# Performance work log

Measured on AMD Instinct MI355X. Metric: run time of the kernel, lower is better.

The kernel has to match this reference:

```python
import jax, jax.numpy as jnp
import numpy as np

LEAKY_SLOPE = 0.01

def bilinear_interpolate(grid, coords):
    # grid: [H, W, C]; coords: [N, 2] in [0,1] (x, y order as in torch code)
    H = grid.shape[0] - 1
    W = grid.shape[1] - 1
    fx = coords[:, 0] * W
    fy = coords[:, 1] * H
    x0 = fx.astype(jnp.int32)
    y0 = fy.astype(jnp.int32)
    xf = jnp.mod(fx, 1.0)
    yf = jnp.mod(fy, 1.0)
    x1 = jnp.minimum(x0 + 1, W)
    y1 = jnp.minimum(y0 + 1, H)
    tl = grid[y0, x0]  # [N, C]
    tr = grid[y0, x1]
    bl = grid[y1, x0]
    br = grid[y1, x1]
    xf = xf[:, None]
    yf = yf[:, None]
    top = (1.0 - xf) * tl + xf * tr
    bot = (1.0 - xf) * bl + xf * br
    return (1.0 - yf) * top + yf * bot


def setup_inputs() -> dict:
    key = jax.random.key(0)
    ks = jax.random.split(key, 10)
    N = 2097152
    pos = jax.random.uniform(ks[0], (N, 2), dtype=jnp.float32)
    dir = jax.random.uniform(ks[1], (N, 2), dtype=jnp.float32)
    pos_grid = jax.random.normal(ks[2], (256, 256, 3), dtype=jnp.float32) * 10.0
    dir_grid = jax.random.normal(ks[3], (256, 256, 3), dtype=jnp.float32) * 10.0
    # Linear layers: PyTorch default init U(-1/sqrt(fan_in), 1/sqrt(fan_in))
    def linear(kw, kb, fan_in, fan_out):
        bound = 1.0 / np.sqrt(fan_in)
        W = jax.random.uniform(kw, (fan_out, fan_in), minval=-bound, maxval=bound, dtype=jnp.float32)
        b = jax.random.uniform(kb, (fan_out,), minval=-bound, maxval=bound, dtype=jnp.float32)
        return W, b
    W1, b1 = linear(ks[4], ks[5], 6, 64)
    W2, b2 = linear(ks[6], ks[7], 64, 64)
    W3, b3 = linear(ks[8], ks[9], 64, 1)
    return {"pos": pos, "dir": dir, "pos_grid": pos_grid, "dir_grid": dir_grid,
            "W1": W1, "b1": b1, "W2": W2, "b2": b2, "W3": W3, "b3": b3}


def reference(pos, dir, pos_grid, dir_grid, W1, b1, W2, b2, W3, b3):
    pos_feat = jax.lax.stop_gradient(bilinear_interpolate(pos_grid, pos))  # .detach() in torch
    dir_feat = jax.lax.stop_gradient(bilinear_interpolate(dir_grid, dir))
    x = jnp.concatenate([pos_feat, dir_feat], axis=1)  # [N, 6]
    x = jax.nn.leaky_relu(x @ W1.T + b1, LEAKY_SLOPE)
    x = jax.nn.leaky_relu(x @ W2.T + b2, LEAKY_SLOPE)
    return jax.nn.sigmoid(x @ W3.T + b3)  # [N, 1]
```

## Files before the change

kernel.cpp:

```cpp
#include <hip/hip_runtime.h>
#include <hip/hip_bf16.h>
#include <math.h>


#define NTHREADS 256
#define NB 4

typedef __attribute__((ext_vector_type(8))) short bf16x8;
typedef __attribute__((ext_vector_type(4))) float f32x4;
typedef __attribute__((ext_vector_type(2))) float f32x2;
typedef __attribute__((ext_vector_type(4))) int i32x4;
typedef __attribute__((ext_vector_type(2))) int i32x2;

static __device__ __forceinline__ short f2bf(float f) {
    return __builtin_bit_cast(short, __float2bfloat16(f));
}
static __device__ __forceinline__ int pk2(float lo, float hi) {
    int r;
    asm("v_cvt_pk_bf16_f32 %0, %1, %2" : "=v"(r) : "v"(lo), "v"(hi));
    return r;
}
static __device__ __forceinline__ float bflo(int u) {
    return __builtin_bit_cast(float, u << 16);
}
static __device__ __forceinline__ float bfhi(int u) {
    return __builtin_bit_cast(float, (int)(u & 0xffff0000));
}
static __device__ __forceinline__ f32x2 leaky2(f32x2 x) {
    return __builtin_elementwise_max(x, x * 0.01f);
}
static __device__ __forceinline__ int selperm(int addr, int pa, int pb,
                                              bool hi) {
    int va = __builtin_amdgcn_ds_bpermute(addr, pa);
    int vb = __builtin_amdgcn_ds_bpermute(addr, pb);
    return hi ? vb : va;
}

__global__ __launch_bounds__(256) void make_patches(
    const float* __restrict__ gP, const float* __restrict__ gD,
    int* __restrict__ outP, int* __restrict__ outD) {
    int gid = blockIdx.x * 256 + threadIdx.x;
    const float* g = (gid < 65536) ? gP : gD;
    int* po = (gid < 65536) ? outP : outD;
    int id = gid & 65535;
    int y0 = id >> 8, x0 = id & 255;
    int x1 = min(x0 + 1, 255), y1 = min(y0 + 1, 255);
    const float* tl = g + (y0 * 256 + x0) * 3;
    const float* tr = g + (y0 * 256 + x1) * 3;
    const float* bl = g + (y1 * 256 + x0) * 3;
    const float* br = g + (y1 * 256 + x1) * 3;
    i32x4 u0;
    i32x2 u1;
    u0[0] = pk2(tl[0], bl[0]);
    u0[1] = pk2(tl[1], bl[1]);
    u0[2] = pk2(tl[2], bl[2]);
    u0[3] = pk2(tr[0], br[0]);
    u1[0] = pk2(tr[1], br[1]);
    u1[1] = pk2(tr[2], br[2]);
    *(i32x4*)(po + id * 8) = u0;
    *(i32x2*)(po + id * 8 + 4) = u1;
}

static __device__ __forceinline__ void patch_issue(
    const int* __restrict__ tab, float px, float py, int* P, float& xf,
    float& yf) {
    float fx = px * 255.0f;
    float fy = py * 255.0f;
    int x0 = (int)fx;
    int y0 = (int)fy;
    xf = fx - floorf(fx);
    yf = fy - floorf(fy);
    int idx = (y0 << 8) | x0;
    i32x4 a = *(const i32x4*)(tab + idx * 8);
    i32x2 b = *(const i32x2*)(tab + idx * 8 + 4);
    P[0] = a[0]; P[1] = a[1]; P[2] = a[2];
    P[3] = a[3]; P[4] = b[0]; P[5] = b[1];
}

static __device__ __forceinline__ void patch_lerp(const int* P, float xf,
                                                  float yf, float* f) {
#pragma unroll
    for (int ch = 0; ch < 3; ++ch) {
        f32x2 L2 = {bflo(P[ch]), bfhi(P[ch])};
        f32x2 R2 = {bflo(P[ch + 3]), bfhi(P[ch + 3])};
        f32x2 v = (R2 - L2) * xf + L2;
        f[ch] = fmaf(yf, v.y - v.x, v.x);
    }
}

__global__ __launch_bounds__(NTHREADS, 3) void mlp_mfma_kernel(
    const float* __restrict__ pos, const float* __restrict__ dir,
    const int* __restrict__ patP, const int* __restrict__ patD,
    const float* __restrict__ W1, const float* __restrict__ b1,
    const float* __restrict__ W2, const float* __restrict__ b2,
    const float* __restrict__ W3, const float* __restrict__ b3,
    float* __restrict__ out) {
    const int lane = threadIdx.x & 63;
    const int c = lane & 15;
    const int q = lane >> 4;

    bf16x8 A1f[4];
#pragma unroll
    for (int mt = 0; mt < 4; ++mt) {
        int f = mt * 16 + c;
        bf16x8 t;
#pragma unroll
        for (int j = 0; j < 8; ++j) {
            float v = 0.0f;
            if (q == 0) {
                if (j < 6) v = W1[f * 6 + j];
                else if (j == 6) v = b1[f];
            }
            t[j] = f2bf(v);
        }
        A1f[mt] = t;
    }
    bf16x8 A2f[2][4];
#pragma unroll
    for (int kt = 0; kt < 2; ++kt)
#pragma unroll
        for (int mt = 0; mt < 4; ++mt) {
            int n2 = mt * 16 + c;
            int k0 = kt * 32 + q * 8;
            bf16x8 t;
#pragma unroll
            for (int j = 0; j < 8; ++j) t[j] = f2bf(W2[n2 * 64 + k0 + j]);
            A2f[kt][mt] = t;
        }
    f32x4 ci[4], w3q[4];
#pragma unroll
    for (int mt = 0; mt < 4; ++mt)
#pragma unroll
        for (int r = 0; r < 4; ++r) {
            ci[mt][r] = b2[mt * 16 + q * 4 + r];
            w3q[mt][r] = W3[mt * 16 + q * 4 + r];
        }
    const float b3s = b3[0];
    const int dbias = 0x3F80;
    const f32x4 zacc = {0.f, 0.f, 0.f, 0.f};

    const int exA = ((((q & 1) * 2) * 16) + c) * 4;
    const int exB = exA + 64;
    const bool hi = (q >= 2);

    const long wave_global = (long)(blockIdx.x * 4) + (threadIdx.x >> 6);
    const long base0 = wave_global * (64L * NB);
    const float2* pos2 = (const float2*)pos;
    const float2* dir2 = (const float2*)dir;

    int PA[12];
    float frA[4];
    float2 cp1, cd1;
    {
        float2 c0p = pos2[base0 + lane], c0d = dir2[base0 + lane];
        cp1 = pos2[base0 + 64 + lane];
        cd1 = dir2[base0 + 64 + lane];
        patch_issue(patP, c0p.x, c0p.y, PA, frA[0], frA[1]);
        patch_issue(patD, c0d.x, c0d.y, PA + 6, frA[2], frA[3]);
    }

#pragma unroll 1
    for (int ib = 0; ib < NB; ++ib) {
        const long base = base0 + ib * 64;

        int d0, d1, d2;
        {
            float feat[6];
            patch_lerp(PA, frA[0], frA[1], feat);
            patch_lerp(PA + 6, frA[2], frA[3], feat + 3);
            d0 = pk2(feat[0], feat[1]);
            d1 = pk2(feat[2], feat[3]);
            d2 = pk2(feat[4], feat[5]);
        }

        patch_issue(patP, cp1.x, cp1.y, PA, frA[0], frA[1]);
        patch_issue(patD, cd1.x, cd1.y, PA + 6, frA[2], frA[3]);
        {
            int mb = min(ib + 2, NB - 1);
            cp1 = pos2[base0 + mb * 64 + lane];
            cd1 = dir2[base0 + mb * 64 + lane];
        }

        float s[4];
#pragma unroll
        for (int pt = 0; pt < 4; ++pt) {
            const int fa = (pt * 16 + c) * 4;
            i32x4 bi;
            bi[0] = __builtin_amdgcn_ds_bpermute(fa, d0);
            bi[1] = __builtin_amdgcn_ds_bpermute(fa, d1);
            bi[2] = __builtin_amdgcn_ds_bpermute(fa, d2);
            bi[3] = dbias;
            bf16x8 bfeat = __builtin_bit_cast(bf16x8, bi);

            f32x4 a1[4];
#pragma unroll
            for (int mt = 0; mt < 4; ++mt)
                a1[mt] = __builtin_amdgcn_mfma_f32_16x16x32_bf16(
                    A1f[mt], bfeat, zacc, 0, 0, 0);

            int Pk[4][2];
#pragma unroll
            for (int mt = 0; mt < 4; ++mt) {
                f32x2 p0 = {a1[mt][0], a1[mt][1]};
                f32x2 p1 = {a1[mt][2], a1[mt][3]};
                p0 = leaky2(p0);
                p1 = leaky2(p1);
                Pk[mt][0] = pk2(p0.x, p0.y);
                Pk[mt][1] = pk2(p1.x, p1.y);
            }

            f32x4 a2[4];
#pragma unroll
            for (int kt = 0; kt < 2; ++kt) {
                i32x4 Q;
                Q[0] = selperm(exA, Pk[2 * kt][0], Pk[2 * kt + 1][0], hi);
                Q[1] = selperm(exA, Pk[2 * kt][1], Pk[2 * kt + 1][1], hi);
                Q[2] = selperm(exB, Pk[2 * kt][0], Pk[2 * kt + 1][0], hi);
                Q[3] = selperm(exB, Pk[2 * kt][1], Pk[2 * kt + 1][1], hi);
                bf16x8 bq = __builtin_bit_cast(bf16x8, Q);
#pragma unroll
                for (int mt = 0; mt < 4; ++mt)
                    a2[mt] = __builtin_amdgcn_mfma_f32_16x16x32_bf16(
                        A2f[kt][mt], bq, kt == 0 ? ci[mt] : a2[mt], 0, 0, 0);
            }

            f32x2 accv = {0.f, 0.f};
#pragma unroll
            for (int mt = 0; mt < 4; ++mt) {
                f32x2 x0 = {a2[mt][0], a2[mt][1]};
                f32x2 x1 = {a2[mt][2], a2[mt][3]};
                x0 = leaky2(x0);
                x1 = leaky2(x1);
                f32x2 w0 = {w3q[mt][0], w3q[mt][1]};
                f32x2 w1 = {w3q[mt][2], w3q[mt][3]};
                accv = x0 * w0 + accv;
                accv = x1 * w1 + accv;
            }
            float tt = accv.x + accv.y;
            tt += __shfl_xor(tt, 16, 64);
            tt += __shfl_xor(tt, 32, 64);
            s[pt] = tt;
        }

        float sa = (q & 1) ? s[1] : s[0];
        float sb = (q & 1) ? s[3] : s[2];
        float v = (q & 2) ? sb : sa;
        v += b3s;
        v = 1.0f / (1.0f + __expf(-v));
        out[base + q * 16 + c] = v;
    }
}

extern "C" void kernel_launch(void* const* d_in, const int* in_sizes, int n_in,
                              void* d_out, int out_size, void* d_ws,
                              size_t ws_size, hipStream_t stream) {
    const float* pos = (const float*)d_in[0];
    const float* dir = (const float*)d_in[1];
    const float* pos_grid = (const float*)d_in[2];
    const float* dir_grid = (const float*)d_in[3];
    const float* W1 = (const float*)d_in[4];
    const float* b1 = (const float*)d_in[5];
    const float* W2 = (const float*)d_in[6];
    const float* b2 = (const float*)d_in[7];
    const float* W3 = (const float*)d_in[8];
    const float* b3 = (const float*)d_in[9];
    float* out = (float*)d_out;

    int* patP = (int*)d_ws;
    int* patD = patP + 65536 * 8;

    make_patches<<<512, 256, 0, stream>>>(pos_grid, dir_grid, patP, patD);

    const int n = in_sizes[0] / 2;
    const int batches = n / 64;
    const int waves = batches / NB;
    const int blocks = waves / 4;

    mlp_mfma_kernel<<<blocks, NTHREADS, 0, stream>>>(
        pos, dir, patP, patD, W1, b1, W2, b2, W3, b3, out);
}
```

Measured before the change: 158.1 us.

## Split bilinear feature gathering into a separate kernel writing packed bf16 features

Moves the grid patch gathers and bilinear interpolation out of the MFMA MLP kernel into a new make_feats kernel. It writes packed bf16 feature vectors (with the bias-one slot) to workspace. The MLP kernel then loads these directly in MFMA B-operand layout, which removes the ds_bpermute shuffles and the latency-bound gathers from the compute loop. The cost is an extra kernel launch plus a write and read of 16 bytes per point (about 32 MB each way) through global memory.

```diff
diff --git a/kernel.cpp b/kernel.cpp
--- a/kernel.cpp
+++ b/kernel.cpp
@@ -88,9 +88,33 @@
     }
 }
 
+__global__ __launch_bounds__(256) void make_feats(
+    const float2* __restrict__ pos2, const float2* __restrict__ dir2,
+    const int* __restrict__ patP, const int* __restrict__ patD,
+    i32x4* __restrict__ featpk, int npts) {
+    int i = blockIdx.x * 256 + threadIdx.x;
+    int stride = gridDim.x * 256;
+#pragma unroll 1
+    for (; i < npts; i += stride) {
+        float2 pp = pos2[i], dd = dir2[i];
+        int P[12];
+        float fr[4];
+        patch_issue(patP, pp.x, pp.y, P, fr[0], fr[1]);
+        patch_issue(patD, dd.x, dd.y, P + 6, fr[2], fr[3]);
+        float feat[6];
+        patch_lerp(P, fr[0], fr[1], feat);
+        patch_lerp(P + 6, fr[2], fr[3], feat + 3);
+        i32x4 dv;
+        dv[0] = pk2(feat[0], feat[1]);
+        dv[1] = pk2(feat[2], feat[3]);
+        dv[2] = pk2(feat[4], feat[5]);
+        dv[3] = 0x3F80;
+        featpk[i] = dv;
+    }
+}
+
 __global__ __launch_bounds__(NTHREADS, 3) void mlp_mfma_kernel(
-    const float* __restrict__ pos, const float* __restrict__ dir,
-    const int* __restrict__ patP, const int* __restrict__ patD,
+    const i32x4* __restrict__ featpk,
     const float* __restrict__ W1, const float* __restrict__ b1,
     const float* __restrict__ W2, const float* __restrict__ b2,
     const float* __restrict__ W3, const float* __restrict__ b3,
@@ -136,7 +160,6 @@
             w3q[mt][r] = W3[mt * 16 + q * 4 + r];
         }
     const float b3s = b3[0];
-    const int dbias = 0x3F80;
     const f32x4 zacc = {0.f, 0.f, 0.f, 0.f};
 
     const int exA = ((((q & 1) * 2) * 16) + c) * 4;
@@ -145,52 +168,26 @@
 
     const long wave_global = (long)(blockIdx.x * 4) + (threadIdx.x >> 6);
     const long base0 = wave_global * (64L * NB);
-    const float2* pos2 = (const float2*)pos;
-    const float2* dir2 = (const float2*)dir;
-
-    int PA[12];
-    float frA[4];
-    float2 cp1, cd1;
-    {
-        float2 c0p = pos2[base0 + lane], c0d = dir2[base0 + lane];
-        cp1 = pos2[base0 + 64 + lane];
-        cd1 = dir2[base0 + 64 + lane];
-        patch_issue(patP, c0p.x, c0p.y, PA, frA[0], frA[1]);
-        patch_issue(patD, c0d.x, c0d.y, PA + 6, frA[2], frA[3]);
-    }
+
+    i32x4 bfc[4];
+#pragma unroll
+    for (int pt = 0; pt < 4; ++pt) bfc[pt] = featpk[base0 + pt * 16 + c];
 
 #pragma unroll 1
     for (int ib = 0; ib < NB; ++ib) {
         const long base = base0 + ib * 64;
 
-        int d0, d1, d2;
+        i32x4 bfn[4];
         {
-            float feat[6];
-            patch_lerp(PA, frA[0], frA[1], feat);
-            patch_lerp(PA + 6, frA[2], frA[3], feat + 3);
-            d0 = pk2(feat[0], feat[1]);
-            d1 = pk2(feat[2], feat[3]);
-            d2 = pk2(feat[4], feat[5]);
-        }
-
-        patch_issue(patP, cp1.x, cp1.y, PA, frA[0], frA[1]);
-        patch_issue(patD, cd1.x, cd1.y, PA + 6, frA[2], frA[3]);
-        {
-            int mb = min(ib + 2, NB - 1);
-            cp1 = pos2[base0 + mb * 64 + lane];
-            cd1 = dir2[base0 + mb * 64 + lane];
+            const long nb = base0 + (long)min(ib + 1, NB - 1) * 64;
+#pragma unroll
+            for (int pt = 0; pt < 4; ++pt) bfn[pt] = featpk[nb + pt * 16 + c];
         }
 
         float s[4];
 #pragma unroll
         for (int pt = 0; pt < 4; ++pt) {
-            const int fa = (pt * 16 + c) * 4;
-            i32x4 bi;
-            bi[0] = __builtin_amdgcn_ds_bpermute(fa, d0);
-            bi[1] = __builtin_amdgcn_ds_bpermute(fa, d1);
-            bi[2] = __builtin_amdgcn_ds_bpermute(fa, d2);
-            bi[3] = dbias;
-            bf16x8 bfeat = __builtin_bit_cast(bf16x8, bi);
+            bf16x8 bfeat = __builtin_bit_cast(bf16x8, bfc[pt]);
 
             f32x4 a1[4];
 #pragma unroll
@@ -248,6 +245,9 @@
         v += b3s;
         v = 1.0f / (1.0f + __expf(-v));
         out[base + q * 16 + c] = v;
+
+#pragma unroll
+        for (int pt = 0; pt < 4; ++pt) bfc[pt] = bfn[pt];
     }
 }
 
@@ -266,16 +266,21 @@
     const float* b3 = (const float*)d_in[9];
     float* out = (float*)d_out;
 
+    const int n = in_sizes[0] / 2;
+
     int* patP = (int*)d_ws;
     int* patD = patP + 65536 * 8;
+    i32x4* featpk = (i32x4*)(patD + 65536 * 8);
 
     make_patches<<<512, 256, 0, stream>>>(pos_grid, dir_grid, patP, patD);
-
-    const int n = in_sizes[0] / 2;
+    make_feats<<<2048, 256, 0, stream>>>((const float2*)pos,
+                                         (const float2*)dir, patP, patD,
+                                         featpk, n);
+
     const int batches = n / 64;
     const int waves = batches / NB;
     const int blocks = waves / 4;
 
-    mlp_mfma_kernel<<<blocks, NTHREADS, 0, stream>>>(
-        pos, dir, patP, patD, W1, b1, W2, b2, W3, b3, out);
-}
+    mlp_mfma_kernel<<<blocks, NTHREADS, 0, stream>>>(featpk, W1, b1, W2, b2,
+                                                     W3, b3, out);
+}
```

Result: slower. 180.2 us (+13.9%).

## Stage layer-1 activations through padded LDS instead of bpermute shuffles

Applied to the files above, without the earlier changes.

Replaces the ds_bpermute-based register exchange between the first and second MFMA layers with a per-wave padded LDS buffer: layer-1 outputs for all four point tiles are written to LDS, then read back as bf16x8 B-fragments for layer 2. The layer-1 and layer-2 MFMAs are batched across all four tiles to give more independent MFMA work. This cuts the 16 bpermutes plus selects per tile, but adds LDS traffic and raises register pressure, so occupancy is lowered to 2 blocks per CU.

```diff
diff --git a/kernel.cpp b/kernel.cpp
--- a/kernel.cpp
+++ b/kernel.cpp
@@ -5,6 +5,8 @@
 
 #define NTHREADS 256
 #define NB 4
+#define LSTRIDE 72
+#define WAVE_L (64 * LSTRIDE)
 
 typedef __attribute__((ext_vector_type(8))) short bf16x8;
 typedef __attribute__((ext_vector_type(4))) float f32x4;
@@ -28,12 +30,6 @@
 }
 static __device__ __forceinline__ f32x2 leaky2(f32x2 x) {
     return __builtin_elementwise_max(x, x * 0.01f);
-}
-static __device__ __forceinline__ int selperm(int addr, int pa, int pb,
-                                              bool hi) {
-    int va = __builtin_amdgcn_ds_bpermute(addr, pa);
-    int vb = __builtin_amdgcn_ds_bpermute(addr, pb);
-    return hi ? vb : va;
 }
 
 __global__ __launch_bounds__(256) void make_patches(
@@ -88,16 +84,19 @@
     }
 }
 
-__global__ __launch_bounds__(NTHREADS, 3) void mlp_mfma_kernel(
+__global__ __launch_bounds__(NTHREADS, 2) void mlp_mfma_kernel(
     const float* __restrict__ pos, const float* __restrict__ dir,
     const int* __restrict__ patP, const int* __restrict__ patD,
     const float* __restrict__ W1, const float* __restrict__ b1,
     const float* __restrict__ W2, const float* __restrict__ b2,
     const float* __restrict__ W3, const float* __restrict__ b3,
     float* __restrict__ out) {
+    __shared__ short lds_L[4 * WAVE_L];
+    const int w = threadIdx.x >> 6;
     const int lane = threadIdx.x & 63;
     const int c = lane & 15;
     const int q = lane >> 4;
+    short* L = lds_L + w * WAVE_L;
 
     bf16x8 A1f[4];
 #pragma unroll
@@ -139,11 +138,7 @@
     const int dbias = 0x3F80;
     const f32x4 zacc = {0.f, 0.f, 0.f, 0.f};
 
-    const int exA = ((((q & 1) * 2) * 16) + c) * 4;
-    const int exB = exA + 64;
-    const bool hi = (q >= 2);
-
-    const long wave_global = (long)(blockIdx.x * 4) + (threadIdx.x >> 6);
+    const long wave_global = (long)(blockIdx.x * 4) + w;
     const long base0 = wave_global * (64L * NB);
     const float2* pos2 = (const float2*)pos;
     const float2* dir2 = (const float2*)dir;
@@ -172,7 +167,6 @@
             d1 = pk2(feat[2], feat[3]);
             d2 = pk2(feat[4], feat[5]);
         }
-
         patch_issue(patP, cp1.x, cp1.y, PA, frA[0], frA[1]);
         patch_issue(patD, cd1.x, cd1.y, PA + 6, frA[2], frA[3]);
         {
@@ -181,7 +175,7 @@
             cd1 = dir2[base0 + mb * 64 + lane];
         }
 
-        float s[4];
+        f32x4 a1[4][4];
 #pragma unroll
         for (int pt = 0; pt < 4; ++pt) {
             const int fa = (pt * 16 + c) * 4;
@@ -191,44 +185,55 @@
             bi[2] = __builtin_amdgcn_ds_bpermute(fa, d2);
             bi[3] = dbias;
             bf16x8 bfeat = __builtin_bit_cast(bf16x8, bi);
-
-            f32x4 a1[4];
 #pragma unroll
             for (int mt = 0; mt < 4; ++mt)
-                a1[mt] = __builtin_amdgcn_mfma_f32_16x16x32_bf16(
+                a1[pt][mt] = __builtin_amdgcn_mfma_f32_16x16x32_bf16(
                     A1f[mt], bfeat, zacc, 0, 0, 0);
-
-            int Pk[4][2];
+        }
+
+#pragma unroll
+        for (int pt = 0; pt < 4; ++pt) {
+            const int row = pt * 16 + c;
 #pragma unroll
             for (int mt = 0; mt < 4; ++mt) {
-                f32x2 p0 = {a1[mt][0], a1[mt][1]};
-                f32x2 p1 = {a1[mt][2], a1[mt][3]};
+                f32x2 p0 = {a1[pt][mt][0], a1[pt][mt][1]};
+                f32x2 p1 = {a1[pt][mt][2], a1[pt][mt][3]};
                 p0 = leaky2(p0);
                 p1 = leaky2(p1);
-                Pk[mt][0] = pk2(p0.x, p0.y);
-                Pk[mt][1] = pk2(p1.x, p1.y);
-            }
-
-            f32x4 a2[4];
-#pragma unroll
-            for (int kt = 0; kt < 2; ++kt) {
-                i32x4 Q;
-                Q[0] = selperm(exA, Pk[2 * kt][0], Pk[2 * kt + 1][0], hi);
-                Q[1] = selperm(exA, Pk[2 * kt][1], Pk[2 * kt + 1][1], hi);
-                Q[2] = selperm(exB, Pk[2 * kt][0], Pk[2 * kt + 1][0], hi);
-                Q[3] = selperm(exB, Pk[2 * kt][1], Pk[2 * kt + 1][1], hi);
-                bf16x8 bq = __builtin_bit_cast(bf16x8, Q);
-#pragma unroll
-                for (int mt = 0; mt < 4; ++mt)
-                    a2[mt] = __builtin_amdgcn_mfma_f32_16x16x32_bf16(
-                        A2f[kt][mt], bq, kt == 0 ? ci[mt] : a2[mt], 0, 0, 0);
-            }
-
+                i32x2 wv;
+                wv[0] = pk2(p0.x, p0.y);
+                wv[1] = pk2(p1.x, p1.y);
+                *(i32x2*)(L + row * LSTRIDE + mt * 16 + q * 4) = wv;
+            }
+        }
+
+        bf16x8 h0[4], h1[4];
+#pragma unroll
+        for (int pt = 0; pt < 4; ++pt) {
+            const int row = pt * 16 + c;
+            h0[pt] = *(const bf16x8*)(L + row * LSTRIDE + q * 8);
+            h1[pt] = *(const bf16x8*)(L + row * LSTRIDE + 32 + q * 8);
+        }
+
+        f32x4 a2[4][4];
+#pragma unroll
+        for (int pt = 0; pt < 4; ++pt)
+#pragma unroll
+            for (int mt = 0; mt < 4; ++mt) {
+                f32x4 t0 = __builtin_amdgcn_mfma_f32_16x16x32_bf16(
+                    A2f[0][mt], h0[pt], ci[mt], 0, 0, 0);
+                a2[pt][mt] = __builtin_amdgcn_mfma_f32_16x16x32_bf16(
+                    A2f[1][mt], h1[pt], t0, 0, 0, 0);
+            }
+
+        float s[4];
+#pragma unroll
+        for (int pt = 0; pt < 4; ++pt) {
             f32x2 accv = {0.f, 0.f};
 #pragma unroll
             for (int mt = 0; mt < 4; ++mt) {
-                f32x2 x0 = {a2[mt][0], a2[mt][1]};
-                f32x2 x1 = {a2[mt][2], a2[mt][3]};
+                f32x2 x0 = {a2[pt][mt][0], a2[pt][mt][1]};
+                f32x2 x1 = {a2[pt][mt][2], a2[pt][mt][3]};
                 x0 = leaky2(x0);
                 x1 = leaky2(x1);
                 f32x2 w0 = {w3q[mt][0], w3q[mt][1]};
```

Result: no change. 156.8 us (-0.8%).
